# Kernel tuning notes

Hardware: AMD Instinct MI355X
Metric: run time of the kernel (lower is better)

The kernel has to match this reference:

```python
import jax, jax.numpy as jnp
import numpy as np

B, NS, NF, D, H = 64, 16, 4096, 128, 256  # batch, n_slots, n_feat, slot_dim, mlp_hidden
EPS_LN = 1e-5
EPS_ATT = 1e-8


def _layernorm(x, g, b):
    mu = x.mean(-1, keepdims=True)
    var = x.var(-1, keepdims=True)
    return (x - mu) / jnp.sqrt(var + EPS_LN) * g + b


def setup_inputs() -> dict:
    key = jax.random.key(0)
    ks = jax.random.split(key, 8)
    s = 0.02  # init scale for weights
    return {
        "t": jnp.zeros((), jnp.float32),
        "slots": jax.random.normal(ks[0], (B, NS, D), jnp.float32),
        "k": jax.random.normal(ks[1], (B, NF, D), jnp.float32),
        "v": jax.random.normal(ks[2], (B, NF, D), jnp.float32),
        "Wq": jax.random.normal(ks[3], (D, D), jnp.float32) * s,           # eqx Linear weight [out,in], no bias
        "ln_slots_g": jnp.ones((D,), jnp.float32),
        "ln_slots_b": jnp.zeros((D,), jnp.float32),
        "W_ih": jax.random.normal(ks[4], (3 * D, D), jnp.float32) * s,     # GRUCell input weights
        "W_hh": jax.random.normal(ks[5], (3 * D, D), jnp.float32) * s,     # GRUCell hidden weights
        "b_ih": jnp.zeros((3 * D,), jnp.float32),
        "b_n": jnp.zeros((D,), jnp.float32),
        "ln_ff_g": jnp.ones((D,), jnp.float32),
        "ln_ff_b": jnp.zeros((D,), jnp.float32),
        "W0": jax.random.normal(ks[6], (H, D), jnp.float32) * s,
        "b0": jnp.zeros((H,), jnp.float32),
        "W1": jax.random.normal(ks[7], (D, H), jnp.float32) * s,
        "b1": jnp.zeros((D,), jnp.float32),
    }


def reference(t, slots, k, v, Wq, ln_slots_g, ln_slots_b,
              W_ih, W_hh, b_ih, b_n, ln_ff_g, ln_ff_b, W0, b0, W1, b1):
    scale = D ** (-0.5)
    # LayerNorm over slot features, then query projection
    slots_norm = _layernorm(slots, ln_slots_g, ln_slots_b)
    q = jnp.einsum('bnd,ed->bne', slots_norm, Wq)                    # [B,NS,D]
    # Doubly-normalized slot attention: softmax over slots (axis=1), renorm over features
    att_logits = jnp.einsum('bnd,bmd->bnm', q, k) * scale            # [B,NS,NF]
    att = jax.nn.softmax(att_logits, axis=1)
    att = att / (att.sum(axis=-1, keepdims=True) + EPS_ATT)
    attended = jnp.einsum('bnm,bmd->bnd', att, v)                    # [B,NS,D]
    # GRUCell (equinox semantics): gates order (reset, input, new)
    igates = jnp.einsum('bnd,ed->bne', attended, W_ih) + b_ih        # [B,NS,3D]
    hgates = jnp.einsum('bnd,ed->bne', slots, W_hh)                  # [B,NS,3D]
    ir, ii, inew = jnp.split(igates, 3, axis=-1)
    hr, hi, hnew = jnp.split(hgates, 3, axis=-1)
    reset = jax.nn.sigmoid(ir + hr)
    inp = jax.nn.sigmoid(ii + hi)
    new = jnp.tanh(inew + reset * (hnew + b_n))
    gru_out = new + inp * (slots - new)                              # [B,NS,D]
    # LayerNorm -> MLP residual
    gru_normed = _layernorm(gru_out, ln_ff_g, ln_ff_b)
    h = jax.nn.relu(jnp.einsum('bnd,hd->bnh', gru_normed, W0) + b0)
    h = jnp.einsum('bnh,dh->bnd', h, W1) + b1
    target = gru_out + h
    return target - slots
```

## Files before the change

kernel.cpp:

```cpp
#include <hip/hip_runtime.h>
#include <hip/hip_bf16.h>
#include <math.h>

#define B_  64
#define NS_ 16
#define NF_ 4096
#define D_  128
#define H_  256


__device__ __forceinline__ float bflo(unsigned int u) { return __uint_as_float(u << 16); }
__device__ __forceinline__ float bfhi(unsigned int u) { return __uint_as_float(u & 0xffff0000u); }

__device__ __forceinline__ unsigned int pk_bf16(float a, float b) {
    unsigned int ua = __float_as_uint(a), ub = __float_as_uint(b);
    ua = (ua + 0x7FFFu + ((ua >> 16) & 1u)) >> 16;
    ub = (ub + 0x7FFFu + ((ub >> 16) & 1u)) >> 16;
    return ua | (ub << 16);
}

__device__ __forceinline__ float dot2_bf16(unsigned int a, unsigned int b, float c) {
    float d;
    asm("v_dot2_f32_bf16 %0, %1, %2, %3" : "=v"(d) : "v"(a), "v"(b), "v"(c));
    return d;
}

__device__ __forceinline__ float dot4(float4 a, float4 b) {
    return a.x * b.x + a.y * b.y + a.z * b.z + a.w * b.w;
}

__global__ __launch_bounds__(128) void k_q(
    const float* __restrict__ slots, const float* __restrict__ Wq,
    const float* __restrict__ lng, const float* __restrict__ lnb,
    unsigned int* __restrict__ q_out, float* __restrict__ acc, float* __restrict__ den) {
    const int b = blockIdx.x;
    const int t = threadIdx.x;
    __shared__ float sl_s[16][128];
    __shared__ float norm_s[16][128];
    __shared__ float st_s[16][8][2];
    __shared__ float mu_s[16], rs_s[16];
    __shared__ float q_s[16][128];

    const float4* sp = (const float4*)(slots + (size_t)b * 2048);
#pragma unroll
    for (int i = 0; i < 4; ++i) {
        int f = i * 128 + t;
        *(float4*)&sl_s[f >> 5][(f & 31) * 4] = sp[f];
    }
    __syncthreads();

    {
        int n = t >> 3, j = t & 7;
        float s1 = 0.f, s2 = 0.f;
#pragma unroll
        for (int d2 = 0; d2 < 16; ++d2) {
            float x = sl_s[n][j * 16 + d2];
            s1 += x; s2 += x * x;
        }
        st_s[n][j][0] = s1; st_s[n][j][1] = s2;
    }
    __syncthreads();
    if (t < 16) {
        float s1 = 0.f, s2 = 0.f;
#pragma unroll
        for (int j = 0; j < 8; ++j) { s1 += st_s[t][j][0]; s2 += st_s[t][j][1]; }
        float mu = s1 * (1.0f / 128.0f);
        float var = s2 * (1.0f / 128.0f) - mu * mu;
        mu_s[t] = mu;
        rs_s[t] = rsqrtf(var + 1e-5f);
    }
    __syncthreads();

    float gl = lng[t], bl = lnb[t];
#pragma unroll
    for (int n = 0; n < 16; ++n)
        norm_s[n][t] = (sl_s[n][t] - mu_s[n]) * rs_s[n] * gl + bl;
    __syncthreads();

    const float4* wq = (const float4*)(Wq + (size_t)t * 128);
    float qn[16];
#pragma unroll
    for (int n = 0; n < 16; ++n) qn[n] = 0.f;
#pragma unroll 4
    for (int j = 0; j < 32; ++j) {
        float4 w4 = wq[j];
#pragma unroll
        for (int n = 0; n < 16; ++n) qn[n] += dot4(w4, *(const float4*)&norm_s[n][4 * j]);
    }
#pragma unroll
    for (int n = 0; n < 16; ++n) q_s[n][t] = qn[n];

    float4 z4 = make_float4(0.f, 0.f, 0.f, 0.f);
    float4* ab = (float4*)(acc + (size_t)b * 2048);
#pragma unroll
    for (int i = 0; i < 4; ++i) ab[i * 128 + t] = z4;
    if (t < 16) den[b * 16 + t] = 0.f;
    __syncthreads();

    unsigned int* qo = q_out + (size_t)b * 1024;
#pragma unroll
    for (int i = 0; i < 8; ++i) {
        int u = i * 128 + t;
        int n = u >> 6, e2 = u & 63;
        qo[n * 64 + e2] = pk_bf16(q_s[n][2 * e2], q_s[n][2 * e2 + 1]);
    }
}

__global__ __launch_bounds__(256) void k_attn(
    const float* __restrict__ kg_, const float* __restrict__ vg_,
    const unsigned int* __restrict__ q_u, float* __restrict__ acc_g, float* __restrict__ denom_g) {
    const int t = threadIdx.x;
    const int w = t >> 6, l = t & 63;
    const int b = blockIdx.y;
    const int n = l & 15;
    const int g = l >> 4;
    const int dcol = t & 127;
    const int nh = t >> 7;

    __shared__ unsigned int lds_u[5632];
    unsigned int* k_s  = lds_u;
    float*        p_s  = (float*)(lds_u + 4352);
    float*        red_d = (float*)(lds_u + 5376);

    uint4 qq[4];
    {
        const uint4* qrow = (const uint4*)q_u + ((b * 16 + n) * 16);
#pragma unroll
        for (int j = 0; j < 4; ++j) qq[j] = qrow[g * 4 + j];
    }

    float acc[8];
#pragma unroll
    for (int i = 0; i < 8; ++i) acc[i] = 0.f;
    float denom_acc = 0.f;

    const size_t mbase = (size_t)b * NF_ + blockIdx.x * 128;
    const float4* kg4 = (const float4*)kg_ + (mbase + w * 16) * 32;
    const float*  vgp = vg_ + mbase * 128 + dcol;

    for (int tile = 0; tile < 2; ++tile) {
        const float4* kp = kg4 + tile * 64 * 32;
#pragma unroll
        for (int c = 0; c < 2; ++c) {
            float4 tmp[4];
#pragma unroll
            for (int i = 0; i < 4; ++i) tmp[i] = kp[(c * 4 + i) * 64 + l];
#pragma unroll
            for (int i = 0; i < 4; ++i) {
                int r = w * 16 + 2 * (c * 4 + i) + (l >> 5);
                *(uint2*)&k_s[r * 68 + 2 * (l & 31)] =
                    make_uint2(pk_bf16(tmp[i].x, tmp[i].y), pk_bf16(tmp[i].z, tmp[i].w));
            }
        }

#pragma unroll
        for (int mi = 0; mi < 16; ++mi) {
            const int row = w * 16 + mi;
            float p0 = 0.f, p1 = 0.f, p2 = 0.f, p3 = 0.f;
#pragma unroll
            for (int j = 0; j < 4; ++j) {
                uint4 kk = *(const uint4*)&k_s[row * 68 + g * 16 + 4 * j];
                p0 = dot2_bf16(kk.x, qq[j].x, p0);
                p1 = dot2_bf16(kk.y, qq[j].y, p1);
                p2 = dot2_bf16(kk.z, qq[j].z, p2);
                p3 = dot2_bf16(kk.w, qq[j].w, p3);
            }
            float x = (p0 + p1) + (p2 + p3);
            x += __shfl_xor(x, 16);
            x += __shfl_xor(x, 32);
            x *= 0.08838834764831845f;
            float e = __expf(x);
            float se = e;
            se += __shfl_xor(se, 1);
            se += __shfl_xor(se, 2);
            se += __shfl_xor(se, 4);
            se += __shfl_xor(se, 8);
            float pv = e * __builtin_amdgcn_rcpf(se);
            if (g == (mi & 3)) {
                denom_acc += pv;
                p_s[row * 16 + n] = pv;
            }
        }
        __syncthreads();

        const float* vt = vgp + (size_t)tile * 64 * 128;
#pragma unroll
        for (int oct = 0; oct < 8; ++oct) {
            float vv[8];
#pragma unroll
            for (int i = 0; i < 8; ++i) vv[i] = vt[(oct * 8 + i) * 128];
#pragma unroll
            for (int i = 0; i < 8; ++i) {
                int m = oct * 8 + i;
                float4 pa = *(const float4*)&p_s[m * 16 + nh * 8];
                float4 pb = *(const float4*)&p_s[m * 16 + nh * 8 + 4];
                acc[0] = fmaf(pa.x, vv[i], acc[0]);
                acc[1] = fmaf(pa.y, vv[i], acc[1]);
                acc[2] = fmaf(pa.z, vv[i], acc[2]);
                acc[3] = fmaf(pa.w, vv[i], acc[3]);
                acc[4] = fmaf(pb.x, vv[i], acc[4]);
                acc[5] = fmaf(pb.y, vv[i], acc[5]);
                acc[6] = fmaf(pb.z, vv[i], acc[6]);
                acc[7] = fmaf(pb.w, vv[i], acc[7]);
            }
        }
        __syncthreads();
    }

    red_d[t] = denom_acc;
    __syncthreads();
    float* base = acc_g + (size_t)b * 2048 + dcol;
#pragma unroll
    for (int i = 0; i < 8; ++i)
        atomicAdd(base + (nh * 8 + i) * 128, acc[i]);
    if (t < 16) {
        float s = 0.f;
#pragma unroll
        for (int j = 0; j < 16; ++j) s += red_d[t + 16 * j];
        atomicAdd(denom_g + b * 16 + t, s);
    }
}

__global__ __launch_bounds__(256) void k_final(
    const float* __restrict__ acc_g, const float* __restrict__ denom_g,
    const float* __restrict__ slots,
    const float* __restrict__ W_ih, const float* __restrict__ W_hh,
    const float* __restrict__ b_ih, const float* __restrict__ b_n,
    const float* __restrict__ ffg, const float* __restrict__ ffb,
    const float* __restrict__ W0, const float* __restrict__ b0,
    const float* __restrict__ W1, const float* __restrict__ b1,
    float* __restrict__ out) {
    const int bn0 = blockIdx.x * 4;
    const int t = threadIdx.x;
    __shared__ float att_s[4][128], slot_s[4][128];
    __shared__ float gates_s[4][4][128];
    __shared__ float gru_s[4][128], gn_s[4][128];
    __shared__ float h_s[4][256];

#pragma unroll
    for (int idx = t; idx < 512; idx += 256) {
        int bi = idx >> 7, d = idx & 127;
        int bn = bn0 + bi;
        float den = denom_g[bn] + 1e-8f;
        att_s[bi][d] = acc_g[(size_t)bn * 128 + d] / den;
        slot_s[bi][d] = slots[(size_t)bn * 128 + d];
    }
    __syncthreads();

    for (int g = t; g < 384; g += 256) {
        const float4* wi = (const float4*)(W_ih + (size_t)g * 128);
        const float4* wh = (const float4*)(W_hh + (size_t)g * 128);
        float si[4] = {0.f, 0.f, 0.f, 0.f}, sh[4] = {0.f, 0.f, 0.f, 0.f};
#pragma unroll 4
        for (int j = 0; j < 32; ++j) {
            float4 wi4 = wi[j], wh4 = wh[j];
#pragma unroll
            for (int bi = 0; bi < 4; ++bi) {
                si[bi] += dot4(wi4, *(const float4*)&att_s[bi][4 * j]);
                sh[bi] += dot4(wh4, *(const float4*)&slot_s[bi][4 * j]);
            }
        }
        float bih = b_ih[g];
        int d = g & 127;
#pragma unroll
        for (int bi = 0; bi < 4; ++bi) {
            if (g < 128)       gates_s[bi][0][d] = si[bi] + sh[bi] + bih;
            else if (g < 256)  gates_s[bi][1][d] = si[bi] + sh[bi] + bih;
            else { gates_s[bi][2][d] = si[bi] + bih; gates_s[bi][3][d] = sh[bi]; }
        }
    }
    __syncthreads();

    {
        int bi = t >> 6, l = t & 63;
        float gr[2], s1 = 0.f, s2 = 0.f;
#pragma unroll
        for (int h = 0; h < 2; ++h) {
            int d = l + 64 * h;
            float rr = 1.f / (1.f + __expf(-gates_s[bi][0][d]));
            float ii = 1.f / (1.f + __expf(-gates_s[bi][1][d]));
            float nv = tanhf(gates_s[bi][2][d] + rr * (gates_s[bi][3][d] + b_n[d]));
            float gru = nv + ii * (slot_s[bi][d] - nv);
            gr[h] = gru;
            gru_s[bi][d] = gru;
            s1 += gru; s2 += gru * gru;
        }
#pragma unroll
        for (int m = 1; m < 64; m <<= 1) { s1 += __shfl_xor(s1, m); s2 += __shfl_xor(s2, m); }
        float mu = s1 * (1.0f / 128.0f);
        float var = s2 * (1.0f / 128.0f) - mu * mu;
        float rstd = rsqrtf(var + 1e-5f);
#pragma unroll
        for (int h = 0; h < 2; ++h) {
            int d = l + 64 * h;
            gn_s[bi][d] = (gr[h] - mu) * rstd * ffg[d] + ffb[d];
        }
    }
    __syncthreads();

    {
        const float4* w0 = (const float4*)(W0 + (size_t)t * 128);
        float s[4] = {0.f, 0.f, 0.f, 0.f};
#pragma unroll 4
        for (int j = 0; j < 32; ++j) {
            float4 w4 = w0[j];
#pragma unroll
            for (int bi = 0; bi < 4; ++bi) s[bi] += dot4(w4, *(const float4*)&gn_s[bi][4 * j]);
        }
        float b0v = b0[t];
#pragma unroll
        for (int bi = 0; bi < 4; ++bi) h_s[bi][t] = fmaxf(s[bi] + b0v, 0.f);
    }
    __syncthreads();

    {
        int dr = t & 127, bp = (t >> 7) * 2;
        const float4* w1 = (const float4*)(W1 + (size_t)dr * 256);
        float s[2] = {0.f, 0.f};
#pragma unroll 4
        for (int j = 0; j < 64; ++j) {
            float4 w4 = w1[j];
#pragma unroll
            for (int u = 0; u < 2; ++u) s[u] += dot4(w4, *(const float4*)&h_s[bp + u][4 * j]);
        }
        float b1v = b1[dr];
#pragma unroll
        for (int u = 0; u < 2; ++u) {
            int bi = bp + u;
            out[(size_t)(bn0 + bi) * 128 + dr] = gru_s[bi][dr] + s[u] + b1v - slot_s[bi][dr];
        }
    }
}

extern "C" void kernel_launch(void* const* d_in, const int* in_sizes, int n_in,
                              void* d_out, int out_size, void* d_ws, size_t ws_size,
                              hipStream_t stream) {
    const float* slots = (const float*)d_in[1];
    const float* k     = (const float*)d_in[2];
    const float* v     = (const float*)d_in[3];
    const float* Wq    = (const float*)d_in[4];
    const float* lng   = (const float*)d_in[5];
    const float* lnb   = (const float*)d_in[6];
    const float* W_ih  = (const float*)d_in[7];
    const float* W_hh  = (const float*)d_in[8];
    const float* b_ih  = (const float*)d_in[9];
    const float* b_n   = (const float*)d_in[10];
    const float* ffg   = (const float*)d_in[11];
    const float* ffb   = (const float*)d_in[12];
    const float* W0    = (const float*)d_in[13];
    const float* b0    = (const float*)d_in[14];
    const float* W1    = (const float*)d_in[15];
    const float* b1    = (const float*)d_in[16];

    char* ws = (char*)d_ws;
    unsigned int* q_u = (unsigned int*)ws;
    float* acc = (float*)(ws + 262144);
    float* den = (float*)(ws + 786432);

    k_q<<<dim3(B_), dim3(128), 0, stream>>>(slots, Wq, lng, lnb, q_u, acc, den);
    k_attn<<<dim3(32, B_), dim3(256), 0, stream>>>(k, v, q_u, acc, den);
    k_final<<<dim3(256), dim3(256), 0, stream>>>(acc, den, slots, W_ih, W_hh,
                                                 b_ih, b_n, ffg, ffb, W0, b0, W1, b1,
                                                 (float*)d_out);
}
```

Measured before the change: 378.8 us.

## Compute attention logits with MFMA bf16 and prefetch V ahead of use

Replaces the per-row v_dot2 bf16 logit loop with a 16x16x32 bf16 MFMA per wave, so each wave computes its 16 slots x 16 features logits in four instructions and does the slot softmax with two cross-lane shuffles. V loads are software-pipelined by double buffering two register groups of eight rows, and the first group is issued before the K staging. The per-slot denominator is reduced with shuffles and atomics, removing the LDS reduction and its barrier. The p_s row stride becomes 20 floats to reduce LDS bank conflicts. The cost is more register pressure from the extra V buffers and a dependence on the MFMA operand layout being correct.

After: 378.3 us. About the same (-0.1%).

```diff
diff --git a/kernel.cpp b/kernel.cpp
--- a/kernel.cpp
+++ b/kernel.cpp
@@ -9,20 +9,18 @@
 #define H_  256
 
 
-__device__ __forceinline__ float bflo(unsigned int u) { return __uint_as_float(u << 16); }
-__device__ __forceinline__ float bfhi(unsigned int u) { return __uint_as_float(u & 0xffff0000u); }
+typedef __attribute__((ext_vector_type(8))) short bf16x8;
+typedef __attribute__((ext_vector_type(4))) float f32x4;
+
+__device__ __forceinline__ bf16x8 as_bf16x8(uint4 u) {
+    union { uint4 u; bf16x8 h; } c; c.u = u; return c.h;
+}
 
 __device__ __forceinline__ unsigned int pk_bf16(float a, float b) {
     unsigned int ua = __float_as_uint(a), ub = __float_as_uint(b);
     ua = (ua + 0x7FFFu + ((ua >> 16) & 1u)) >> 16;
     ub = (ub + 0x7FFFu + ((ub >> 16) & 1u)) >> 16;
     return ua | (ub << 16);
-}
-
-__device__ __forceinline__ float dot2_bf16(unsigned int a, unsigned int b, float c) {
-    float d;
-    asm("v_dot2_f32_bf16 %0, %1, %2, %3" : "=v"(d) : "v"(a), "v"(b), "v"(c));
-    return d;
 }
 
 __device__ __forceinline__ float dot4(float4 a, float4 b) {
@@ -112,113 +110,129 @@
     const int t = threadIdx.x;
     const int w = t >> 6, l = t & 63;
     const int b = blockIdx.y;
-    const int n = l & 15;
-    const int g = l >> 4;
+    const int lm = l & 15;
+    const int g  = l >> 4;
     const int dcol = t & 127;
     const int nh = t >> 7;
 
     __shared__ unsigned int lds_u[5632];
-    unsigned int* k_s  = lds_u;
-    float*        p_s  = (float*)(lds_u + 4352);
-    float*        red_d = (float*)(lds_u + 5376);
-
-    uint4 qq[4];
-    {
-        const uint4* qrow = (const uint4*)q_u + ((b * 16 + n) * 16);
-#pragma unroll
-        for (int j = 0; j < 4; ++j) qq[j] = qrow[g * 4 + j];
+    unsigned int* k_s = lds_u;
+    float*        p_s = (float*)(lds_u + 4352);
+
+    uint4 qA[4];
+    {
+        const uint4* qb = (const uint4*)q_u + ((b * 16 + lm) * 16);
+#pragma unroll
+        for (int kk = 0; kk < 4; ++kk) qA[kk] = qb[kk * 4 + g];
     }
 
     float acc[8];
 #pragma unroll
     for (int i = 0; i < 8; ++i) acc[i] = 0.f;
-    float denom_acc = 0.f;
+    float dn[4] = {0.f, 0.f, 0.f, 0.f};
 
     const size_t mbase = (size_t)b * NF_ + blockIdx.x * 128;
     const float4* kg4 = (const float4*)kg_ + (mbase + w * 16) * 32;
     const float*  vgp = vg_ + mbase * 128 + dcol;
 
-    for (int tile = 0; tile < 2; ++tile) {
-        const float4* kp = kg4 + tile * 64 * 32;
-#pragma unroll
-        for (int c = 0; c < 2; ++c) {
-            float4 tmp[4];
-#pragma unroll
-            for (int i = 0; i < 4; ++i) tmp[i] = kp[(c * 4 + i) * 64 + l];
-#pragma unroll
-            for (int i = 0; i < 4; ++i) {
-                int r = w * 16 + 2 * (c * 4 + i) + (l >> 5);
-                *(uint2*)&k_s[r * 68 + 2 * (l & 31)] =
-                    make_uint2(pk_bf16(tmp[i].x, tmp[i].y), pk_bf16(tmp[i].z, tmp[i].w));
+    for (int sub = 0; sub < 2; ++sub) {
+        const float* vt = vgp + (size_t)sub * 64 * 128;
+
+        float vva[8], vvb[8];
+#pragma unroll
+        for (int i = 0; i < 8; ++i) vva[i] = vt[i * 128];
+
+        const float4* kp = kg4 + sub * 64 * 32;
+#pragma unroll
+        for (int c = 0; c < 4; ++c) {
+            float4 t0 = kp[(2 * c) * 64 + l];
+            float4 t1 = kp[(2 * c + 1) * 64 + l];
+            int r0 = w * 16 + 2 * (2 * c) + (l >> 5);
+            int r1 = w * 16 + 2 * (2 * c + 1) + (l >> 5);
+            *(uint2*)&k_s[r0 * 68 + 2 * (l & 31)] =
+                make_uint2(pk_bf16(t0.x, t0.y), pk_bf16(t0.z, t0.w));
+            *(uint2*)&k_s[r1 * 68 + 2 * (l & 31)] =
+                make_uint2(pk_bf16(t1.x, t1.y), pk_bf16(t1.z, t1.w));
+        }
+
+        f32x4 sacc = {0.f, 0.f, 0.f, 0.f};
+#pragma unroll
+        for (int kk = 0; kk < 4; ++kk) {
+            uint4 kb = *(const uint4*)&k_s[(w * 16 + lm) * 68 + kk * 16 + g * 4];
+            sacc = __builtin_amdgcn_mfma_f32_16x16x32_bf16(
+                as_bf16x8(qA[kk]), as_bf16x8(kb), sacc, 0, 0, 0);
+        }
+        const float scale = 0.08838834764831845f;
+        float e0 = __expf(sacc[0] * scale);
+        float e1 = __expf(sacc[1] * scale);
+        float e2 = __expf(sacc[2] * scale);
+        float e3 = __expf(sacc[3] * scale);
+        float se = (e0 + e1) + (e2 + e3);
+        se += __shfl_xor(se, 16);
+        se += __shfl_xor(se, 32);
+        float rse = __builtin_amdgcn_rcpf(se);
+        float4 pv4 = make_float4(e0 * rse, e1 * rse, e2 * rse, e3 * rse);
+        dn[0] += pv4.x; dn[1] += pv4.y; dn[2] += pv4.z; dn[3] += pv4.w;
+        *(float4*)&p_s[(w * 16 + lm) * 20 + g * 4] = pv4;
+        __syncthreads();
+
+#pragma unroll
+        for (int op = 0; op < 4; ++op) {
+            const int octA = 2 * op, octB = 2 * op + 1;
+#pragma unroll
+            for (int i = 0; i < 8; ++i) vvb[i] = vt[(octB * 8 + i) * 128];
+#pragma unroll
+            for (int i = 0; i < 8; ++i) {
+                int m = octA * 8 + i;
+                float4 pa = *(const float4*)&p_s[m * 20 + nh * 8];
+                float4 pb = *(const float4*)&p_s[m * 20 + nh * 8 + 4];
+                float vvi = vva[i];
+                acc[0] = fmaf(pa.x, vvi, acc[0]);
+                acc[1] = fmaf(pa.y, vvi, acc[1]);
+                acc[2] = fmaf(pa.z, vvi, acc[2]);
+                acc[3] = fmaf(pa.w, vvi, acc[3]);
+                acc[4] = fmaf(pb.x, vvi, acc[4]);
+                acc[5] = fmaf(pb.y, vvi, acc[5]);
+                acc[6] = fmaf(pb.z, vvi, acc[6]);
+                acc[7] = fmaf(pb.w, vvi, acc[7]);
             }
-        }
-
-#pragma unroll
-        for (int mi = 0; mi < 16; ++mi) {
-            const int row = w * 16 + mi;
-            float p0 = 0.f, p1 = 0.f, p2 = 0.f, p3 = 0.f;
-#pragma unroll
-            for (int j = 0; j < 4; ++j) {
-                uint4 kk = *(const uint4*)&k_s[row * 68 + g * 16 + 4 * j];
-                p0 = dot2_bf16(kk.x, qq[j].x, p0);
-                p1 = dot2_bf16(kk.y, qq[j].y, p1);
-                p2 = dot2_bf16(kk.z, qq[j].z, p2);
-                p3 = dot2_bf16(kk.w, qq[j].w, p3);
+            if (op < 3) {
+#pragma unroll
+                for (int i = 0; i < 8; ++i) vva[i] = vt[((octB + 1) * 8 + i) * 128];
             }
-            float x = (p0 + p1) + (p2 + p3);
-            x += __shfl_xor(x, 16);
-            x += __shfl_xor(x, 32);
-            x *= 0.08838834764831845f;
-            float e = __expf(x);
-            float se = e;
-            se += __shfl_xor(se, 1);
-            se += __shfl_xor(se, 2);
-            se += __shfl_xor(se, 4);
-            se += __shfl_xor(se, 8);
-            float pv = e * __builtin_amdgcn_rcpf(se);
-            if (g == (mi & 3)) {
-                denom_acc += pv;
-                p_s[row * 16 + n] = pv;
+#pragma unroll
+            for (int i = 0; i < 8; ++i) {
+                int m = octB * 8 + i;
+                float4 pa = *(const float4*)&p_s[m * 20 + nh * 8];
+                float4 pb = *(const float4*)&p_s[m * 20 + nh * 8 + 4];
+                float vvi = vvb[i];
+                acc[0] = fmaf(pa.x, vvi, acc[0]);
+                acc[1] = fmaf(pa.y, vvi, acc[1]);
+                acc[2] = fmaf(pa.z, vvi, acc[2]);
+                acc[3] = fmaf(pa.w, vvi, acc[3]);
+                acc[4] = fmaf(pb.x, vvi, acc[4]);
+                acc[5] = fmaf(pb.y, vvi, acc[5]);
+                acc[6] = fmaf(pb.z, vvi, acc[6]);
+                acc[7] = fmaf(pb.w, vvi, acc[7]);
             }
         }
         __syncthreads();
-
-        const float* vt = vgp + (size_t)tile * 64 * 128;
-#pragma unroll
-        for (int oct = 0; oct < 8; ++oct) {
-            float vv[8];
-#pragma unroll
-            for (int i = 0; i < 8; ++i) vv[i] = vt[(oct * 8 + i) * 128];
-#pragma unroll
-            for (int i = 0; i < 8; ++i) {
-                int m = oct * 8 + i;
-                float4 pa = *(const float4*)&p_s[m * 16 + nh * 8];
-                float4 pb = *(const float4*)&p_s[m * 16 + nh * 8 + 4];
-                acc[0] = fmaf(pa.x, vv[i], acc[0]);
-                acc[1] = fmaf(pa.y, vv[i], acc[1]);
-                acc[2] = fmaf(pa.z, vv[i], acc[2]);
-                acc[3] = fmaf(pa.w, vv[i], acc[3]);
-                acc[4] = fmaf(pb.x, vv[i], acc[4]);
-                acc[5] = fmaf(pb.y, vv[i], acc[5]);
-                acc[6] = fmaf(pb.z, vv[i], acc[6]);
-                acc[7] = fmaf(pb.w, vv[i], acc[7]);
-            }
-        }
-        __syncthreads();
-    }
-
-    red_d[t] = denom_acc;
-    __syncthreads();
+    }
+
+#pragma unroll
+    for (int m = 1; m <= 8; m <<= 1) {
+#pragma unroll
+        for (int r = 0; r < 4; ++r) dn[r] += __shfl_xor(dn[r], m);
+    }
+    if (lm == 0) {
+#pragma unroll
+        for (int r = 0; r < 4; ++r)
+            atomicAdd(denom_g + b * 16 + g * 4 + r, dn[r]);
+    }
     float* base = acc_g + (size_t)b * 2048 + dcol;
 #pragma unroll
     for (int i = 0; i < 8; ++i)
         atomicAdd(base + (nh * 8 + i) * 128, acc[i]);
-    if (t < 16) {
-        float s = 0.f;
-#pragma unroll
-        for (int j = 0; j < 16; ++j) s += red_d[t + 16 * j];
-        atomicAdd(denom_g + b * 16 + t, s);
-    }
 }
 
 __global__ __launch_bounds__(256) void k_final(
```
